# Kernel tuning notes

Hardware: AMD Instinct MI355X
Metric: run time of the kernel (lower is better)

The kernel has to match this reference:

```python
import jax, jax.numpy as jnp
import numpy as np

B, S, D, H = 4, 1024, 512, 8
DH = D // H
INNER = 1536  # int(2*D*4/3) rounded up to multiple of 256


def setup_inputs() -> dict:
    key = jax.random.key(0)
    ks = jax.random.split(key, 16)
    g = lambda i, shape, fan: (jax.random.normal(ks[i], shape, jnp.float32) / np.sqrt(fan))
    return {
        "x": jax.random.normal(ks[0], (B, S, D), jnp.float32),
        "Wq": g(1, (D, D), D), "bq": jnp.zeros((D,), jnp.float32),
        "Wkv": g(2, (D, 2 * D), D), "bkv": jnp.zeros((2 * D,), jnp.float32),
        "Wo": g(3, (D, D), D), "bo": jnp.zeros((D,), jnp.float32),
        "rms_w": jnp.ones((D,), jnp.float32),
        "l1": g(4, (D, INNER), D), "l2": g(5, (D, INNER), D), "l3": g(6, (INNER, D), INNER),
        "in_w": jnp.ones((D,), jnp.float32), "in_b": jnp.zeros((D,), jnp.float32),
    }


def rms_norm(x, w, eps=1e-6):
    return x * jax.lax.rsqrt(jnp.mean(x * x, axis=-1, keepdims=True) + eps) * w


def instance_norm(x, w, b, eps=1e-5):
    # InstanceNorm1d(affine=True) over the sequence dim per (batch, channel); x: [B,S,D]
    m = jnp.mean(x, axis=1, keepdims=True)
    v = jnp.mean((x - m) ** 2, axis=1, keepdims=True)
    return (x - m) * jax.lax.rsqrt(v + eps) * w + b


def sparse_sdpa(q, k, v):
    # q,k,v: [B,H,S,DH]
    b, h, s, dh = q.shape
    scores = jnp.einsum("bhsd,bhtd->bhst", q, k) / np.sqrt(dh).astype(np.float32)
    w = jax.nn.softmax(scores, axis=-1)
    kk = s // 2
    _, idx = jax.lax.top_k(w, kk)  # [B,H,S,kk]
    bi = jnp.arange(b)[:, None, None, None]
    hi = jnp.arange(h)[None, :, None, None]
    ri = jnp.arange(s)[None, None, :, None]
    mask = jnp.zeros_like(w).at[bi, hi, ri, idx].set(1.0)
    masked = jnp.where(mask > 0, w, 0.0)  # zeros (not -inf), per original
    aw = jax.nn.softmax(masked, axis=-1)
    return jnp.einsum("bhst,bhtd->bhsd", aw, v)


def reference(x, Wq, bq, Wkv, bkv, Wo, bo, rms_w, l1, l2, l3, in_w, in_b):
    # attention: q from Wq, k/v from packed Wkv ('b s (two h d)')
    q = (x @ Wq + bq).reshape(B, S, H, DH).transpose(0, 2, 1, 3)
    kv = (x @ Wkv + bkv).reshape(B, S, 2, H, DH)
    k = kv[:, :, 0].transpose(0, 2, 1, 3)
    v = kv[:, :, 1].transpose(0, 2, 1, 3)
    o = sparse_sdpa(q, k, v)
    attn_out = o.transpose(0, 2, 1, 3).reshape(B, S, D) @ Wo + bo
    h_hat = rms_norm(x + attn_out, rms_w)
    ffn = (jax.nn.silu(h_hat @ l1) * (h_hat @ l2)) @ l3
    return instance_norm(h_hat + ffn, in_w, in_b)
```

## Files before the change

### kernel.cpp

```cpp
#include <hip/hip_runtime.h>
#include <stdint.h>

#define B_ 4
#define S_ 1024
#define D_ 512
#define H_ 8
#define DH_ 64
#define INNER_ 1536
#define M_ (B_*S_)

typedef unsigned short u16;
typedef __attribute__((ext_vector_type(8))) short sh8;
typedef __attribute__((ext_vector_type(8))) _Float16 h8;
typedef __attribute__((ext_vector_type(2))) _Float16 h2f;
typedef __attribute__((ext_vector_type(4))) float f32x4;

typedef __attribute__((address_space(1))) const void cgv;
typedef __attribute__((address_space(3))) void lv;
__device__ __forceinline__ void gl_lds16(const void* g, void* l) {
  __builtin_amdgcn_global_load_lds((cgv*)g, (lv*)l, 16, 0, 0);
}
#define WAITVM(N) __builtin_amdgcn_s_waitcnt(0x0F70 | (N))

__device__ __forceinline__ float bf2f(u16 u) {
  union { unsigned int i; float f; } v; v.i = ((unsigned int)u) << 16; return v.f;
}
__device__ __forceinline__ u16 f2bf(float f) {
  union { float f; unsigned int i; } v; v.f = f;
  unsigned int u = v.i;
  return (u16)((u + 0x7FFFu + ((u >> 16) & 1u)) >> 16);
}
__device__ __forceinline__ u16 f2h(float f) {
  _Float16 h = (_Float16)f;
  return *(u16*)&h;
}

__global__ __launch_bounds__(256) void prep_all(
    const float* __restrict__ Wq, const float* __restrict__ Wkv,
    const float* __restrict__ Wo, const float* __restrict__ l1,
    const float* __restrict__ l2, const float* __restrict__ l3,
    const float* __restrict__ x,
    u16* __restrict__ Wt1, u16* __restrict__ Wot,
    u16* __restrict__ W12t, u16* __restrict__ l3t,
    u16* __restrict__ xb)
{
  int i = blockIdx.x;
  if (i >= 832) {
    int e = ((i - 832) * 256 + threadIdx.x) * 4;
    float4 v = *(const float4*)(x + e);
    uint2 o;
    o.x = (unsigned int)f2bf(v.x) | ((unsigned int)f2bf(v.y) << 16);
    o.y = (unsigned int)f2bf(v.z) | ((unsigned int)f2bf(v.w) << 16);
    *(uint2*)(xb + e) = o;
    return;
  }
  const float* in; u16* outp; int K, N, bx, by, rs = 1, ra = 0;
  if (i < 64)       { in = Wq;  outp = Wt1;              K = 512;  N = 512;           bx = i & 7;  by = i >> 3; }
  else if (i < 192) { in = Wkv; outp = Wt1 + 512 * 512;  K = 512;  N = 1024; i -= 64; bx = i & 15; by = i >> 4; }
  else if (i < 256) { in = Wo;  outp = Wot;              K = 512;  N = 512;  i -= 192; bx = i & 7;  by = i >> 3; }
  else if (i < 448) { in = l1;  outp = W12t;             K = 512;  N = 1536; i -= 256; bx = i % 24; by = i / 24; rs = 2; ra = 0; }
  else if (i < 640) { in = l2;  outp = W12t;             K = 512;  N = 1536; i -= 448; bx = i % 24; by = i / 24; rs = 2; ra = 1; }
  else              { in = l3;  outp = l3t;              K = 1536; N = 512;  i -= 640; bx = i & 7;  by = i >> 3; }

  __shared__ u16 tile[64][65];
  int tx = threadIdx.x & 63, ty = threadIdx.x >> 6;
  int n0 = bx * 64, k0 = by * 64;
  #pragma unroll
  for (int t = 0; t < 16; t++) {
    int k = ty + t * 4;
    tile[k][tx] = f2bf(in[(size_t)(k0 + k) * N + n0 + tx]);
  }
  __syncthreads();
  #pragma unroll
  for (int t = 0; t < 8; t++) {
    int n = (threadIdx.x >> 5) + t * 8;
    int c = (threadIdx.x & 31) * 2;
    unsigned int val = (unsigned int)tile[c][n] | ((unsigned int)tile[c + 1][n] << 16);
    *(unsigned int*)&outp[(size_t)((n0 + n) * rs + ra) * K + k0 + c] = val;
  }
}

template<int EPI>
__global__ __launch_bounds__(256) void gemm_bt(
    const u16* __restrict__ A, const u16* __restrict__ Bt,
    int M, int N, int K,
    const float* __restrict__ bias0, const float* __restrict__ bias1,
    u16* __restrict__ outU,
    u16* __restrict__ qo, u16* __restrict__ ko_, u16* __restrict__ vto)
{
  __shared__ u16 As[2 * 64 * 32];
  __shared__ u16 Bs[2 * 128 * 32];
  int tid = threadIdx.x;
  int gx = blockIdx.x, gy = blockIdx.y;
  int l = tid & 63, w = tid >> 6;
  int l15 = l & 15, quad = l >> 4;
  int wm = (w >> 1) * 32, wn = (w & 1) * 64;
  f32x4 acc[2][4] = {};

  const u16* Ag = A  + (size_t)(gy * 64  + (tid >> 2)) * K + (tid & 3) * 8;
  const u16* Bg = Bt + (size_t)(gx * 128 + (tid >> 2)) * K + (tid & 3) * 8;

  auto stage = [&](int t, int buf) {
    int ko2 = t * 32;
    gl_lds16(Ag + ko2,                  &As[buf * 2048 + tid * 8]);
    gl_lds16(Bg + ko2,                  &Bs[buf * 4096 + tid * 8]);
    gl_lds16(Bg + (size_t)64 * K + ko2, &Bs[buf * 4096 + 2048 + tid * 8]);
  };

  const int nT = K >> 5;
  stage(0, 0);
  __syncthreads();
  int cur = 0;
  for (int t = 0; t < nT; t++) {
    if (t + 1 < nT) stage(t + 1, cur ^ 1);
    sh8 af[2], bfr[4];
    #pragma unroll
    for (int mi = 0; mi < 2; mi++)
      af[mi] = *(const sh8*)&As[cur * 2048 + (wm + mi * 16 + l15) * 32 + quad * 8];
    #pragma unroll
    for (int ni = 0; ni < 4; ni++)
      bfr[ni] = *(const sh8*)&Bs[cur * 4096 + (wn + ni * 16 + l15) * 32 + quad * 8];
    #pragma unroll
    for (int mi = 0; mi < 2; mi++)
      #pragma unroll
      for (int ni = 0; ni < 4; ni++)
        acc[mi][ni] = __builtin_amdgcn_mfma_f32_16x16x32_bf16(af[mi], bfr[ni], acc[mi][ni], 0, 0, 0);
    __syncthreads();
    cur ^= 1;
  }

  #pragma unroll
  for (int mi = 0; mi < 2; mi++) {
    #pragma unroll
    for (int ni = 0; ni < 4; ni++) {
      if (EPI == 1) {
        int growb = gy * 64 + wm + mi * 16 + quad * 4;
        int gcol = gx * 128 + wn + ni * 16 + l15;
        int b = growb >> 10, s0 = growb & 1023;
        if (gcol < 512) {
          int h = gcol >> 6, dh = gcol & 63;
          float bi = bias0[gcol];
          #pragma unroll
          for (int r = 0; r < 4; r++)
            qo[(((size_t)b * H_ + h) * S_ + s0 + r) * DH_ + dh] = f2h(acc[mi][ni][r] + bi);
        } else {
          int n2 = gcol - 512;
          int two = n2 >> 9, h = (n2 >> 6) & 7, dh = n2 & 63;
          float bi = bias1[n2];
          if (two == 0) {
            #pragma unroll
            for (int r = 0; r < 4; r++)
              ko_[(((size_t)b * H_ + h) * S_ + s0 + r) * DH_ + dh] = f2h(acc[mi][ni][r] + bi);
          } else {
            uint2 pk;
            pk.x = (unsigned int)f2h(acc[mi][ni][0] + bi) | ((unsigned int)f2h(acc[mi][ni][1] + bi) << 16);
            pk.y = (unsigned int)f2h(acc[mi][ni][2] + bi) | ((unsigned int)f2h(acc[mi][ni][3] + bi) << 16);
            *(uint2*)&vto[(((size_t)b * H_ + h) * DH_ + dh) * S_ + s0] = pk;
          }
        }
      } else {
        #pragma unroll
        for (int r = 0; r < 4; r++) {
          int grow = gy * 64 + wm + mi * 16 + quad * 4 + r;
          int gcol = gx * 128 + wn + ni * 16 + l15;
          float v = acc[mi][ni][r];
          float vp = __shfl_xor(v, 1);
          if ((l15 & 1) == 0) {
            float a = v, b = vp;
            float gv = a / (1.f + __expf(-a)) * b;
            outU[(size_t)grow * (N >> 1) + (gcol >> 1)] = f2bf(gv);
          }
        }
      }
    }
  }
}

template<int EPI>
__global__ __launch_bounds__(256) void gemm_n64(
    const u16* __restrict__ A, const u16* __restrict__ Bt,
    int M, int N, int K,
    const float* __restrict__ bias0, const float* __restrict__ auxF,
    const u16* __restrict__ auxH, float* __restrict__ outF,
    float* __restrict__ part, u16* __restrict__ outH)
{
  __shared__ u16 sbuf[4 * 3 * 2048];
  __shared__ float ss1[4][2][16], ss2[4][2][16];
  int tid = threadIdx.x;
  int gx = blockIdx.x, gy = blockIdx.y;
  int l = tid & 63, w = tid >> 6;
  int l15 = l & 15, quad = l >> 4;
  int wm = (w >> 1) * 32, wn = (w & 1) * 32;
  int lr = l >> 2, lc = l & 3;
  f32x4 acc[2][2] = {};

  u16* wb = sbuf + (size_t)w * (3 * 2048);
  const u16* Aw = A  + (size_t)(gy * 64 + wm + lr) * K + lc * 8;
  const u16* Bw = Bt + (size_t)(gx * 64 + wn + lr) * K + lc * 8;

  auto stage = [&](int t, int buf) {
    u16* d = wb + buf * 2048;
    const u16* a = Aw + t * 32;
    gl_lds16(a,                  d + l * 8);
    gl_lds16(a + (size_t)16 * K, d + 512  + l * 8);
    const u16* b2 = Bw + t * 32;
    gl_lds16(b2,                  d + 1024 + l * 8);
    gl_lds16(b2 + (size_t)16 * K, d + 1536 + l * 8);
  };

  int nT = K >> 5;
  stage(0, 0);
  stage(1, 1);
  int cb = 0;
  for (int t = 0; t < nT; t++) {
    int nb = (cb == 2) ? 0 : cb + 1;
    int pb = (nb == 2) ? 0 : nb + 1;
    if (t + 2 < nT)      { stage(t + 2, pb); WAITVM(8); }
    else if (t + 1 < nT) { WAITVM(4); }
    else                 { WAITVM(0); }
    const u16* d = wb + cb * 2048;
    sh8 af[2], bfr[2];
    #pragma unroll
    for (int mi = 0; mi < 2; mi++)
      af[mi] = *(const sh8*)&d[(mi * 16 + l15) * 32 + quad * 8];
    #pragma unroll
    for (int ni = 0; ni < 2; ni++)
      bfr[ni] = *(const sh8*)&d[1024 + (ni * 16 + l15) * 32 + quad * 8];
    #pragma unroll
    for (int mi = 0; mi < 2; mi++)
      #pragma unroll
      for (int ni = 0; ni < 2; ni++)
        acc[mi][ni] = __builtin_amdgcn_mfma_f32_16x16x32_bf16(af[mi], bfr[ni], acc[mi][ni], 0, 0, 0);
    cb = nb;
  }

  float cs1[2] = {0.f, 0.f}, cs2[2] = {0.f, 0.f};
  #pragma unroll
  for (int mi = 0; mi < 2; mi++) {
    #pragma unroll
    for (int ni = 0; ni < 2; ni++) {
      #pragma unroll
      for (int r = 0; r < 4; r++) {
        int grow = gy * 64 + wm + mi * 16 + quad * 4 + r;
        int gcol = gx * 64 + wn + ni * 16 + l15;
        float v = acc[mi][ni][r];
        if (EPI == 2) {
          v += bias0[gcol] + auxF[(size_t)grow * N + gcol];
          outH[(size_t)grow * N + gcol] = f2bf(v);
        } else {
          v += bf2f(auxH[(size_t)grow * N + gcol]);
          outF[(size_t)grow * N + gcol] = v;
          cs1[ni] += v; cs2[ni] += v * v;
        }
      }
    }
  }
  if (EPI == 4) {
    #pragma unroll
    for (int ni = 0; ni < 2; ni++) {
      cs1[ni] += __shfl_xor(cs1[ni], 16); cs1[ni] += __shfl_xor(cs1[ni], 32);
      cs2[ni] += __shfl_xor(cs2[ni], 16); cs2[ni] += __shfl_xor(cs2[ni], 32);
    }
    if (l < 16) {
      ss1[w][0][l15] = cs1[0]; ss1[w][1][l15] = cs1[1];
      ss2[w][0][l15] = cs2[0]; ss2[w][1][l15] = cs2[1];
    }
    __syncthreads();
    if (tid < 64) {
      int wsel = (tid >> 5) & 1, ni = (tid >> 4) & 1, cl = tid & 15;
      float s1 = ss1[wsel][ni][cl] + ss1[wsel + 2][ni][cl];
      float s2 = ss2[wsel][ni][cl] + ss2[wsel + 2][ni][cl];
      int col = gx * 64 + wsel * 32 + ni * 16 + cl;
      int b = gy >> 4, seg = gy & 15;
      float2 p; p.x = s1; p.y = s2;
      *(float2*)&part[((size_t)(b * 512 + col) * 16 + seg) * 2] = p;
    }
  }
}

#define RSTRIDE 1032
#define STAGE_H (16 * RSTRIDE)
__global__ __launch_bounds__(256, 3) void attn_kernel(
    const u16* __restrict__ q, const u16* __restrict__ kk,
    const u16* __restrict__ vt, u16* __restrict__ attn)
{
  __shared__ u16 scb[16 * RSTRIDE + 4 * 2048 + 256];
  float* sums = (float*)(scb + 16 * RSTRIDE + 4 * 2048);

  int tid = threadIdx.x;
  int l = tid & 63, w = tid >> 6;
  int l15 = l & 15, quad = l >> 4;
  int blk = blockIdx.x;
  int xcd = blk & 7, li = blk >> 3;
  int bh = xcd * 4 + (li & 3);
  int r0 = (li >> 2) << 4;

  const u16* qb = q  + ((size_t)bh * S_ + r0) * DH_;
  const u16* kb = kk + (size_t)bh * S_ * DH_;
  const u16* vb = vt + (size_t)bh * DH_ * S_;

  int ws = STAGE_H + w * 2048;
  int lr = l >> 2, lc = l & 3;

  {
    const u16* s0 = kb + (size_t)((w << 4) + lr) * DH_ + lc * 8;
    gl_lds16(s0,      &scb[ws + l * 8]);
    gl_lds16(s0 + 32, &scb[ws + 512 + l * 8]);
    const u16* s1 = kb + (size_t)(((1 << 6) | (w << 4)) + lr) * DH_ + lc * 8;
    gl_lds16(s1,      &scb[ws + 1024 + l * 8]);
    gl_lds16(s1 + 32, &scb[ws + 1536 + l * 8]);
  }

  h8 aq0 = *(const h8*)(qb + l15 * DH_ + quad * 8);
  h8 aq1 = *(const h8*)(qb + l15 * DH_ + 32 + quad * 8);

  uint32_t kv[32];
  float S1 = 0.f, S2 = 0.f;
  #pragma unroll
  for (int i = 0; i < 16; i++) {
    if (i + 2 < 16) {
      int t0n = (((i + 2) << 2) | w) << 4;
      const u16* src = kb + (size_t)(t0n + lr) * DH_ + lc * 8;
      int sb = ws + ((i + 2) & 1) * 1024;
      gl_lds16(src,      &scb[sb + l * 8]);
      gl_lds16(src + 32, &scb[sb + 512 + l * 8]);
    }
    if (i + 2 < 16) { WAITVM(4); } else if (i + 1 < 16) { WAITVM(2); } else { WAITVM(0); }
    int sb = ws + (i & 1) * 1024;
    h8 bk0 = *(const h8*)&scb[sb + l15 * 32 + quad * 8];
    h8 bk1 = *(const h8*)&scb[sb + 512 + l15 * 32 + quad * 8];
    f32x4 s4 = {};
    s4 = __builtin_amdgcn_mfma_f32_16x16x32_f16(bk0, aq0, s4, 0, 0, 0);
    s4 = __builtin_amdgcn_mfma_f32_16x16x32_f16(bk1, aq1, s4, 0, 0, 0);
    float e0 = exp2f(fmaf(s4[0], 0.18033688f, -11.5415603f));
    float e1 = exp2f(fmaf(s4[1], 0.18033688f, -11.5415603f));
    float e2 = exp2f(fmaf(s4[2], 0.18033688f, -11.5415603f));
    float e3 = exp2f(fmaf(s4[3], 0.18033688f, -11.5415603f));
    S1 += e0 + e1 + e2 + e3;
    S2 += e0 * e0 + e1 * e1 + e2 * e2 + e3 * e3;
    h2f p0; p0[0] = (_Float16)e0; p0[1] = (_Float16)e1;
    h2f p1; p1[0] = (_Float16)e2; p1[1] = (_Float16)e3;
    kv[2 * i]     = __builtin_bit_cast(uint32_t, p0);
    kv[2 * i + 1] = __builtin_bit_cast(uint32_t, p1);
  }
  S1 += __shfl_xor(S1, 16); S1 += __shfl_xor(S1, 32);
  S2 += __shfl_xor(S2, 16); S2 += __shfl_xor(S2, 32);
  if (l < 16) {
    sums[(w * 16 + l15) * 2]     = S1;
    sums[(w * 16 + l15) * 2 + 1] = S2;
  }
  __syncthreads();

  int n0 = w << 4;
  const u16* vsrc = vb + (size_t)(n0 + lr) * S_ + lc * 8;
  gl_lds16(vsrc,      &scb[ws + l * 8]);
  gl_lds16(vsrc + 32, &scb[ws + 512 + l * 8]);
  gl_lds16(vsrc + 64, &scb[ws + 1024 + l * 8]);

  float Z1 = 0.f, S2t = 0.f;
  #pragma unroll
  for (int ww = 0; ww < 4; ww++) {
    Z1  += sums[(ww * 16 + l15) * 2];
    S2t += sums[(ww * 16 + l15) * 2 + 1];
  }
  float invZ1 = 1.0f / Z1;
  float Z2 = 1025.0f + 0.5f * S2t * invZ1 * invZ1;
  float invZ2 = 1.0f / Z2;

  _Float16 izh = (_Float16)invZ1;
  h2f izv; izv[0] = izh; izv[1] = izh;
  _Float16 z2h = (_Float16)invZ2;
  h2f z2v; z2v[0] = z2h; z2v[1] = z2h;
  h2f onev; onev[0] = (_Float16)1.f; onev[1] = (_Float16)1.f;
  h2f c2v;  c2v[0] = (_Float16)0.5f; c2v[1] = (_Float16)0.5f;
  h2f c6v;  c6v[0] = (_Float16)(1.f/6.f); c6v[1] = (_Float16)(1.f/6.f);
  #pragma unroll
  for (int i = 0; i < 16; i++) {
    int t0 = ((i << 2) | w) << 4;
    uint2 ov;
    #pragma unroll
    for (int hwd = 0; hwd < 2; hwd++) {
      h2f e = __builtin_bit_cast(h2f, kv[2 * i + hwd]);
      h2f wv = e * izv;
      h2f p = wv * c6v + c2v;
      h2f qq = wv * p + onev;
      h2f cm1 = wv * qq;
      h2f cp = cm1 * z2v + z2v;
      (&ov.x)[hwd] = __builtin_bit_cast(uint32_t, cp);
    }
    *(uint2*)(scb + l15 * RSTRIDE + t0 + quad * 4) = ov;
  }
  __syncthreads();

  const u16* crow = scb + l15 * RSTRIDE;
  f32x4 oacc = {};
  #pragma unroll
  for (int kt = 0; kt < 32; kt++) {
    if (kt + 3 < 32)
      gl_lds16(vsrc + (kt + 3) * 32, &scb[ws + ((kt + 3) & 3) * 512 + l * 8]);
    if (kt < 29) { WAITVM(3); } else if (kt == 29) { WAITVM(2); }
    else if (kt == 30) { WAITVM(1); } else { WAITVM(0); }
    h8 ca = *(const h8*)(crow + kt * 32 + quad * 8);
    h8 vv = *(const h8*)&scb[ws + (kt & 3) * 512 + l15 * 32 + quad * 8];
    oacc = __builtin_amdgcn_mfma_f32_16x16x32_f16(ca, vv, oacc, 0, 0, 0);
  }
  int b = bh >> 3, hh = bh & 7;
  #pragma unroll
  for (int r = 0; r < 4; r++) {
    int rr = quad * 4 + r;
    attn[((size_t)b * S_ + r0 + rr) * D_ + hh * DH_ + n0 + l15] = f2bf(oacc[r]);
  }
}

__global__ __launch_bounds__(128) void rms_kernel(const u16* __restrict__ in,
                                                  const float* __restrict__ w,
                                                  u16* __restrict__ out) {
  int row = blockIdx.x;
  int tid = threadIdx.x;
  int d0 = tid * 4;
  uint2 pv = *(const uint2*)(in + (size_t)row * D_ + d0);
  float v0 = bf2f((u16)(pv.x & 0xffff)), v1 = bf2f((u16)(pv.x >> 16));
  float v2 = bf2f((u16)(pv.y & 0xffff)), v3 = bf2f((u16)(pv.y >> 16));
  float s = v0 * v0 + v1 * v1 + v2 * v2 + v3 * v3;
  #pragma unroll
  for (int d = 1; d < 64; d <<= 1) s += __shfl_xor(s, d);
  __shared__ float red[2];
  if ((tid & 63) == 0) red[tid >> 6] = s;
  __syncthreads();
  s = red[0] + red[1];
  float rs = rsqrtf(s * (1.0f / 512.0f) + 1e-6f);
  float4 wv = *(const float4*)(w + d0);
  uint2 o;
  o.x = (unsigned int)f2bf(v0 * rs * wv.x) | ((unsigned int)f2bf(v1 * rs * wv.y) << 16);
  o.y = (unsigned int)f2bf(v2 * rs * wv.z) | ((unsigned int)f2bf(v3 * rs * wv.w) << 16);
  *(uint2*)(out + (size_t)row * D_ + d0) = o;
}

__global__ __launch_bounds__(256) void inorm_stats2(const float* __restrict__ part,
                                                    float* __restrict__ stats) {
  int idx = blockIdx.x * 256 + threadIdx.x;
  float s1 = 0.f, s2 = 0.f;
  #pragma unroll
  for (int i = 0; i < 16; i++) {
    float2 p = *(const float2*)&part[((size_t)idx * 16 + i) * 2];
    s1 += p.x; s2 += p.y;
  }
  float m = s1 * (1.f / 1024.f);
  float var = s2 * (1.f / 1024.f) - m * m;
  stats[idx * 2]     = m;
  stats[idx * 2 + 1] = rsqrtf(var + 1e-5f);
}

__global__ __launch_bounds__(256) void inorm_apply(const float* __restrict__ y,
                                                   const float* __restrict__ stats,
                                                   const float* __restrict__ w,
                                                   const float* __restrict__ bias,
                                                   float* __restrict__ out) {
  int row = blockIdx.x;
  int b = row >> 10;
  int tid = threadIdx.x;
  int d0 = tid * 2;
  float4 st = *(const float4*)(stats + ((size_t)b * D_ + d0) * 2);
  float2 y2 = *(const float2*)(y + (size_t)row * D_ + d0);
  float2 w2 = *(const float2*)(w + d0);
  float2 b2 = *(const float2*)(bias + d0);
  float2 o;
  o.x = (y2.x - st.x) * st.y * w2.x + b2.x;
  o.y = (y2.y - st.z) * st.w * w2.y + b2.y;
  *(float2*)(out + (size_t)row * D_ + d0) = o;
}

extern "C" void kernel_launch(void* const* d_in, const int* in_sizes, int n_in,
                              void* d_out, int out_size, void* d_ws, size_t ws_size,
                              hipStream_t stream) {
  const float* x    = (const float*)d_in[0];
  const float* Wq   = (const float*)d_in[1];
  const float* bq   = (const float*)d_in[2];
  const float* Wkv  = (const float*)d_in[3];
  const float* bkv  = (const float*)d_in[4];
  const float* Wo   = (const float*)d_in[5];
  const float* bo   = (const float*)d_in[6];
  const float* rmsw = (const float*)d_in[7];
  const float* l1   = (const float*)d_in[8];
  const float* l2   = (const float*)d_in[9];
  const float* l3   = (const float*)d_in[10];
  const float* inw  = (const float*)d_in[11];
  const float* inb  = (const float*)d_in[12];
  float* out = (float*)d_out;

  char* ws = (char*)d_ws;
  size_t off = 0;
  auto alloc = [&](size_t n) { char* p = ws + off; off += (n + 255) & ~(size_t)255; return p; };
  u16*  xb   = (u16*) alloc((size_t)M_ * D_ * 2);
  u16*  Wt1  = (u16*) alloc((size_t)1536 * 512 * 2);
  u16*  Wot  = (u16*) alloc((size_t)512 * 512 * 2);
  u16*  W12t = (u16*) alloc((size_t)3072 * 512 * 2);
  u16*  l3t  = (u16*) alloc((size_t)512 * 1536 * 2);
  u16*  qb   = (u16*) alloc((size_t)M_ * D_ * 2);
  u16*  kb   = (u16*) alloc((size_t)M_ * D_ * 2);
  u16*  vtb  = (u16*) alloc((size_t)M_ * D_ * 2);
  u16*  attn = (u16*) alloc((size_t)M_ * D_ * 2);
  u16*  tmpH = (u16*) alloc((size_t)M_ * D_ * 2);
  float* tmpF = (float*)alloc((size_t)M_ * D_ * 4);
  u16*  hhat = (u16*) alloc((size_t)M_ * D_ * 2);
  u16*  g    = (u16*) alloc((size_t)M_ * INNER_ * 2);
  float* part  = (float*)alloc((size_t)B_ * D_ * 16 * 2 * 4);
  float* stats = (float*)alloc((size_t)B_ * D_ * 2 * 4);

  prep_all<<<2880, 256, 0, stream>>>(Wq, Wkv, Wo, l1, l2, l3, x,
                                     Wt1, Wot, W12t, l3t, xb);

  gemm_bt<1><<<dim3(12, 64), 256, 0, stream>>>(xb, Wt1, M_, 1536, 512,
      bq, bkv, nullptr, qb, kb, vtb);

  attn_kernel<<<2048, 256, 0, stream>>>(qb, kb, vtb, attn);

  gemm_n64<2><<<dim3(8, 64), 256, 0, stream>>>(attn, Wot, M_, 512, 512,
      bo, x, nullptr, nullptr, nullptr, tmpH);

  rms_kernel<<<4096, 128, 0, stream>>>(tmpH, rmsw, hhat);

  gemm_bt<3><<<dim3(24, 64), 256, 0, stream>>>(hhat, W12t, M_, 3072, 512,
      nullptr, nullptr, g, nullptr, nullptr, nullptr);

  gemm_n64<4><<<dim3(8, 64), 256, 0, stream>>>(g, l3t, M_, 512, 1536,
      nullptr, nullptr, hhat, tmpF, part, nullptr);

  inorm_stats2<<<8, 256, 0, stream>>>(part, stats);
  inorm_apply<<<4096, 256, 0, stream>>>(tmpF, stats, inw, inb, out);
}
```

Before: 212.7 us.

## Fold RMSNorm into neighboring GEMMs and drop the standalone rms kernel

Row sum-of-squares for RMSNorm is now computed in the Wo GEMM epilogue as per-block partials, reduced by a tiny rms_stats kernel. The rms weight is folded into l1/l2 during weight prep. The per-row scale is applied in the gated-FFN GEMM epilogue and in the l3 residual epilogue, so the normalized hhat buffer is no longer materialized. The residual now reads x as bf16 (xb) rather than fp32, which removes a full-tensor pass and an extra write/read at the cost of slightly lower residual precision.

```diff
diff --git a/kernel.cpp b/kernel.cpp
--- a/kernel.cpp
+++ b/kernel.cpp
@@ -39,7 +39,7 @@
     const float* __restrict__ Wq, const float* __restrict__ Wkv,
     const float* __restrict__ Wo, const float* __restrict__ l1,
     const float* __restrict__ l2, const float* __restrict__ l3,
-    const float* __restrict__ x,
+    const float* __restrict__ x, const float* __restrict__ rmsw,
     u16* __restrict__ Wt1, u16* __restrict__ Wot,
     u16* __restrict__ W12t, u16* __restrict__ l3t,
     u16* __restrict__ xb)
@@ -55,11 +55,12 @@
     return;
   }
   const float* in; u16* outp; int K, N, bx, by, rs = 1, ra = 0;
+  const float* sc = nullptr;
   if (i < 64)       { in = Wq;  outp = Wt1;              K = 512;  N = 512;           bx = i & 7;  by = i >> 3; }
   else if (i < 192) { in = Wkv; outp = Wt1 + 512 * 512;  K = 512;  N = 1024; i -= 64; bx = i & 15; by = i >> 4; }
   else if (i < 256) { in = Wo;  outp = Wot;              K = 512;  N = 512;  i -= 192; bx = i & 7;  by = i >> 3; }
-  else if (i < 448) { in = l1;  outp = W12t;             K = 512;  N = 1536; i -= 256; bx = i % 24; by = i / 24; rs = 2; ra = 0; }
-  else if (i < 640) { in = l2;  outp = W12t;             K = 512;  N = 1536; i -= 448; bx = i % 24; by = i / 24; rs = 2; ra = 1; }
+  else if (i < 448) { in = l1;  outp = W12t;             K = 512;  N = 1536; i -= 256; bx = i % 24; by = i / 24; rs = 2; ra = 0; sc = rmsw; }
+  else if (i < 640) { in = l2;  outp = W12t;             K = 512;  N = 1536; i -= 448; bx = i % 24; by = i / 24; rs = 2; ra = 1; sc = rmsw; }
   else              { in = l3;  outp = l3t;              K = 1536; N = 512;  i -= 640; bx = i & 7;  by = i >> 3; }
 
   __shared__ u16 tile[64][65];
@@ -68,7 +69,9 @@
   #pragma unroll
   for (int t = 0; t < 16; t++) {
     int k = ty + t * 4;
-    tile[k][tx] = f2bf(in[(size_t)(k0 + k) * N + n0 + tx]);
+    float vv = in[(size_t)(k0 + k) * N + n0 + tx];
+    if (sc) vv *= sc[k0 + k];
+    tile[k][tx] = f2bf(vv);
   }
   __syncthreads();
   #pragma unroll
@@ -159,15 +162,17 @@
           }
         }
       } else {
+        int growb = gy * 64 + wm + mi * 16 + quad * 4;
+        float4 r4 = *(const float4*)(bias0 + growb);
+        float rsa[4] = {r4.x, r4.y, r4.z, r4.w};
         #pragma unroll
         for (int r = 0; r < 4; r++) {
-          int grow = gy * 64 + wm + mi * 16 + quad * 4 + r;
+          int grow = growb + r;
           int gcol = gx * 128 + wn + ni * 16 + l15;
-          float v = acc[mi][ni][r];
-          float vp = __shfl_xor(v, 1);
+          float vs = acc[mi][ni][r] * rsa[r];
+          float vp = __shfl_xor(vs, 1);
           if ((l15 & 1) == 0) {
-            float a = v, b = vp;
-            float gv = a / (1.f + __expf(-a)) * b;
+            float gv = vs / (1.f + __expf(-vs)) * vp;
             outU[(size_t)grow * (N >> 1) + (gcol >> 1)] = f2bf(gv);
           }
         }
@@ -186,6 +191,7 @@
 {
   __shared__ u16 sbuf[4 * 3 * 2048];
   __shared__ float ss1[4][2][16], ss2[4][2][16];
+  __shared__ float ssr[4][32];
   int tid = threadIdx.x;
   int gx = blockIdx.x, gy = blockIdx.y;
   int l = tid & 63, w = tid >> 6;
@@ -235,8 +241,20 @@
   }
 
   float cs1[2] = {0.f, 0.f}, cs2[2] = {0.f, 0.f};
+  float sq[2][4] = {};
+  float rw[2];
+  if (EPI == 4) {
+    rw[0] = auxF[gx * 64 + wn + l15];
+    rw[1] = auxF[gx * 64 + wn + 16 + l15];
+  }
   #pragma unroll
   for (int mi = 0; mi < 2; mi++) {
+    float rsa[4];
+    if (EPI == 4) {
+      int growb = gy * 64 + wm + mi * 16 + quad * 4;
+      float4 r4 = *(const float4*)(bias0 + growb);
+      rsa[0] = r4.x; rsa[1] = r4.y; rsa[2] = r4.z; rsa[3] = r4.w;
+    }
     #pragma unroll
     for (int ni = 0; ni < 2; ni++) {
       #pragma unroll
@@ -245,14 +263,40 @@
         int gcol = gx * 64 + wn + ni * 16 + l15;
         float v = acc[mi][ni][r];
         if (EPI == 2) {
-          v += bias0[gcol] + auxF[(size_t)grow * N + gcol];
+          v += bias0[gcol] + bf2f(auxH[(size_t)grow * N + gcol]);
           outH[(size_t)grow * N + gcol] = f2bf(v);
+          sq[mi][r] += v * v;
         } else {
-          v += bf2f(auxH[(size_t)grow * N + gcol]);
+          v += bf2f(auxH[(size_t)grow * N + gcol]) * rsa[r] * rw[ni];
           outF[(size_t)grow * N + gcol] = v;
           cs1[ni] += v; cs2[ni] += v * v;
         }
       }
+    }
+  }
+  if (EPI == 2) {
+    #pragma unroll
+    for (int mi = 0; mi < 2; mi++)
+      #pragma unroll
+      for (int r = 0; r < 4; r++) {
+        float s = sq[mi][r];
+        s += __shfl_xor(s, 1); s += __shfl_xor(s, 2);
+        s += __shfl_xor(s, 4); s += __shfl_xor(s, 8);
+        sq[mi][r] = s;
+      }
+    if (l15 == 0) {
+      #pragma unroll
+      for (int mi = 0; mi < 2; mi++)
+        #pragma unroll
+        for (int r = 0; r < 4; r++)
+          ssr[w][mi * 16 + quad * 4 + r] = sq[mi][r];
+    }
+    __syncthreads();
+    if (tid < 64) {
+      int rr = tid;
+      int wb2 = (rr >> 5) << 1;
+      float p = ssr[wb2][rr & 31] + ssr[wb2 + 1][rr & 31];
+      part[((size_t)(gy * 64 + rr)) * 8 + gx] = p;
     }
   }
   if (EPI == 4) {
@@ -276,6 +320,15 @@
       *(float2*)&part[((size_t)(b * 512 + col) * 16 + seg) * 2] = p;
     }
   }
+}
+
+__global__ __launch_bounds__(256) void rms_stats(const float* __restrict__ part,
+                                                 float* __restrict__ rsb) {
+  int idx = blockIdx.x * 256 + threadIdx.x;
+  float s = 0.f;
+  #pragma unroll
+  for (int i = 0; i < 8; i++) s += part[(size_t)idx * 8 + i];
+  rsb[idx] = rsqrtf(s * (1.0f / 512.0f) + 1e-6f);
 }
 
 #define RSTRIDE 1032
@@ -412,30 +465,6 @@
   }
 }
 
-__global__ __launch_bounds__(128) void rms_kernel(const u16* __restrict__ in,
-                                                  const float* __restrict__ w,
-                                                  u16* __restrict__ out) {
-  int row = blockIdx.x;
-  int tid = threadIdx.x;
-  int d0 = tid * 4;
-  uint2 pv = *(const uint2*)(in + (size_t)row * D_ + d0);
-  float v0 = bf2f((u16)(pv.x & 0xffff)), v1 = bf2f((u16)(pv.x >> 16));
-  float v2 = bf2f((u16)(pv.y & 0xffff)), v3 = bf2f((u16)(pv.y >> 16));
-  float s = v0 * v0 + v1 * v1 + v2 * v2 + v3 * v3;
-  #pragma unroll
-  for (int d = 1; d < 64; d <<= 1) s += __shfl_xor(s, d);
-  __shared__ float red[2];
-  if ((tid & 63) == 0) red[tid >> 6] = s;
-  __syncthreads();
-  s = red[0] + red[1];
-  float rs = rsqrtf(s * (1.0f / 512.0f) + 1e-6f);
-  float4 wv = *(const float4*)(w + d0);
-  uint2 o;
-  o.x = (unsigned int)f2bf(v0 * rs * wv.x) | ((unsigned int)f2bf(v1 * rs * wv.y) << 16);
-  o.y = (unsigned int)f2bf(v2 * rs * wv.z) | ((unsigned int)f2bf(v3 * rs * wv.w) << 16);
-  *(uint2*)(out + (size_t)row * D_ + d0) = o;
-}
-
 __global__ __launch_bounds__(256) void inorm_stats2(const float* __restrict__ part,
                                                     float* __restrict__ stats) {
   int idx = blockIdx.x * 256 + threadIdx.x;
@@ -502,12 +531,13 @@
   u16*  attn = (u16*) alloc((size_t)M_ * D_ * 2);
   u16*  tmpH = (u16*) alloc((size_t)M_ * D_ * 2);
   float* tmpF = (float*)alloc((size_t)M_ * D_ * 4);
-  u16*  hhat = (u16*) alloc((size_t)M_ * D_ * 2);
   u16*  g    = (u16*) alloc((size_t)M_ * INNER_ * 2);
+  float* rspart = (float*)alloc((size_t)M_ * 8 * 4);
+  float* rsb    = (float*)alloc((size_t)M_ * 4);
   float* part  = (float*)alloc((size_t)B_ * D_ * 16 * 2 * 4);
   float* stats = (float*)alloc((size_t)B_ * D_ * 2 * 4);
 
-  prep_all<<<2880, 256, 0, stream>>>(Wq, Wkv, Wo, l1, l2, l3, x,
+  prep_all<<<2880, 256, 0, stream>>>(Wq, Wkv, Wo, l1, l2, l3, x, rmsw,
                                      Wt1, Wot, W12t, l3t, xb);
 
   gemm_bt<1><<<dim3(12, 64), 256, 0, stream>>>(xb, Wt1, M_, 1536, 512,
@@ -516,15 +546,15 @@
   attn_kernel<<<2048, 256, 0, stream>>>(qb, kb, vtb, attn);
 
   gemm_n64<2><<<dim3(8, 64), 256, 0, stream>>>(attn, Wot, M_, 512, 512,
-      bo, x, nullptr, nullptr, nullptr, tmpH);
-
-  rms_kernel<<<4096, 128, 0, stream>>>(tmpH, rmsw, hhat);
-
-  gemm_bt<3><<<dim3(24, 64), 256, 0, stream>>>(hhat, W12t, M_, 3072, 512,
-      nullptr, nullptr, g, nullptr, nullptr, nullptr);
+      bo, nullptr, xb, nullptr, rspart, tmpH);
+
+  rms_stats<<<16, 256, 0, stream>>>(rspart, rsb);
+
+  gemm_bt<3><<<dim3(24, 64), 256, 0, stream>>>(tmpH, W12t, M_, 3072, 512,
+      rsb, nullptr, g, nullptr, nullptr, nullptr);
 
   gemm_n64<4><<<dim3(8, 64), 256, 0, stream>>>(g, l3t, M_, 512, 1536,
-      nullptr, nullptr, hhat, tmpF, part, nullptr);
+      rsb, rmsw, tmpH, tmpF, part, nullptr);
 
   inorm_stats2<<<8, 256, 0, stream>>>(part, stats);
   inorm_apply<<<4096, 256, 0, stream>>>(tmpF, stats, inw, inb, out);
```

New measurement: 224.5 us. +5.6%, slower.
